# Kernel tuning notes

Measured on AMD Instinct MI355X. Metric: run time of the kernel, lower is better.

## Reference

```python
import jax, jax.numpy as jnp
import numpy as np

B, C, H, W = 4, 256, 48, 48
KD, NH, AR = 32, 8, 4
D = AR * KD            # 128, value dim per head
NHKD = NH * KD         # 256
DH = NH * D            # 1024
EPS = 1e-5


def _bn(y, g, b):
    # BN with fresh running stats (mean=0, var=1): y*g/sqrt(1+eps)+b, over channel dim
    s = g / jnp.sqrt(jnp.float32(1.0) + EPS)
    return y * s[None, :, None] + b[None, :, None]


def setup_inputs() -> dict:
    key = jax.random.key(0)
    ks = jax.random.split(key, 13)
    w = lambda k, sh: jax.random.normal(k, sh, jnp.float32) * 0.05
    g = lambda k, sh: 1.0 + jax.random.normal(k, sh, jnp.float32) * 0.05
    return {
        "x": jax.random.normal(ks[0], (B, C, H, W), jnp.float32),
        "wq": w(ks[1], (NHKD, C)), "gq": g(ks[2], (NHKD,)), "bq": w(ks[3], (NHKD,)),
        "wk": w(ks[4], (NHKD, C)), "gk": g(ks[5], (NHKD,)), "bk": w(ks[6], (NHKD,)),
        "wv": w(ks[7], (DH, C)),   "gv": g(ks[8], (DH,)),   "bv": w(ks[9], (DH,)),
        "wp": w(ks[10], (C, DH)),  "gp": g(ks[11], (C,)),   "bp": w(ks[12], (C,)),
    }


def reference(x, wq, gq, bq, wk, gk, bk, wv, gv, bv, wp, gp, bp):
    b, c, h, w = x.shape
    n = h * w
    xf = x.reshape(b, c, n)                                   # [B,C,N]
    # 1x1 conv == channel matmul, then BN
    q = _bn(jnp.einsum('oc,bcn->bon', wq, xf), gq, bq).reshape(b, NH, KD, n)
    k = _bn(jnp.einsum('oc,bcn->bon', wk, xf), gk, bk).reshape(b, NH, KD, n)
    v = _bn(jnp.einsum('oc,bcn->bon', wv, xf), gv, bv).reshape(b, NH, D, n)
    # NOTE: original forward does NOT apply self.scale
    attn = jax.nn.softmax(jnp.einsum('bhkn,bhkm->bhnm', q, k), axis=-1)  # [B,H,N,N]
    xx = jnp.einsum('bhnm,bhdm->bhdn', attn, v).reshape(b, DH, n)        # [B,DH,N]
    out = _bn(jnp.einsum('oc,bcn->bon', wp, jax.nn.relu(xx)), gp, bp)
    return out.reshape(b, c, h, w)
```

## Files before the change

### kernel.cpp

```cpp
#include <hip/hip_runtime.h>

#define BB 4
#define C 256
#define HW 2304
#define NH 8
#define KD 32
#define D 128
#define DH 1024
#define MQ 256

typedef unsigned short bf16u;
typedef __attribute__((ext_vector_type(8))) short short8;
typedef __attribute__((ext_vector_type(4))) short bfx4;
typedef __attribute__((ext_vector_type(4))) float f32x4;
typedef __attribute__((ext_vector_type(4))) unsigned ux4;
typedef __attribute__((ext_vector_type(2))) unsigned ux2;

union U8 { ux4 u; short8 s; };

__device__ __forceinline__ bf16u f2b(float f) {
    unsigned u = __float_as_uint(f);
    return (bf16u)((u + 0x7fffu + ((u >> 16) & 1u)) >> 16);
}
__device__ __forceinline__ unsigned pkb(float a, float b) {
    return __builtin_amdgcn_perm(__float_as_uint(b) + 0x8000u,
                                 __float_as_uint(a) + 0x8000u, 0x07060302u);
}

__device__ __forceinline__ void glds16(const bf16u* g, bf16u* l) {
    __builtin_amdgcn_global_load_lds(
        (const __attribute__((address_space(1))) unsigned int*)g,
        (__attribute__((address_space(3))) unsigned int*)l,
        16, 0, 0);
}

#define MFMA32 __builtin_amdgcn_mfma_f32_16x16x32_bf16

__global__ __launch_bounds__(256) void prepx(
    const float* __restrict__ wq, const float* __restrict__ wk, const float* __restrict__ wv,
    const float* __restrict__ gq, const float* __restrict__ bq,
    const float* __restrict__ gk, const float* __restrict__ bk,
    const float* __restrict__ gv, const float* __restrict__ bv,
    const float* __restrict__ x,
    bf16u* __restrict__ WcT, float* __restrict__ biasc, bf16u* __restrict__ xT)
{
    __shared__ float tile[64][68];
    const float rs = rsqrtf(1.0f + 1e-5f);
    const float L2E = 1.4426950408889634f;
    const int t = threadIdx.x, blk = blockIdx.x;
    if (blk < 192) {
        const int idx = (blk*256 + t) * 8;
        const int row = idx >> 8;
        const int k   = idx & 255;
        const float* src; float sc;
        if (row < 256)      { src = wq + idx;            sc = gq[row]*rs*L2E; }
        else if (row < 512) { src = wk + (idx - 65536);  sc = gk[row-256]*rs; }
        else                { src = wv + (idx - 131072); sc = gv[row-512]*rs; }
        float4 a = *(const float4*)(src);
        float4 c = *(const float4*)(src + 4);
        ux4 v;
        v.x = pkb(a.x*sc, a.y*sc); v.y = pkb(a.z*sc, a.w*sc);
        v.z = pkb(c.x*sc, c.y*sc); v.w = pkb(c.z*sc, c.w*sc);
        const size_t dst = (size_t)((row>>7)*8 + (k>>5))*4096
                         + (size_t)((row&127)*4 + ((k&31)>>3))*8;
        *(ux4*)(WcT + dst) = v;
    } else if (blk == 192) {
        #pragma unroll
        for (int kk = 0; kk < 6; ++kk) {
            const int r = kk*256 + t;
            float v;
            if (r < 256)      v = bq[r] * L2E;
            else if (r < 512) v = bk[r - 256];
            else              v = bv[r - 512];
            biasc[r] = v;
        }
    } else {
        const int idx = blk - 193;
        const int c0 = (idx & 3) * 64, n0 = ((idx >> 2) % 36) * 64, b = idx / 144;
        const float* xb = x + (size_t)b * C * HW;
        #pragma unroll
        for (int rr = 0; rr < 4; ++rr) {
            const int cl = rr*16 + (t >> 4);
            float4 v = *(const float4*)(xb + (size_t)(c0 + cl) * HW + n0 + (t & 15)*4);
            tile[cl][(t&15)*4+0] = v.x; tile[cl][(t&15)*4+1] = v.y;
            tile[cl][(t&15)*4+2] = v.z; tile[cl][(t&15)*4+3] = v.w;
        }
        __syncthreads();
        const int nl = t >> 2, ch = t & 3;
        short8 v0, v1;
        #pragma unroll
        for (int kk = 0; kk < 8; ++kk) v0[kk] = (short)f2b(tile[ch*16+kk][nl]);
        #pragma unroll
        for (int kk = 0; kk < 8; ++kk) v1[kk] = (short)f2b(tile[ch*16+8+kk][nl]);
        bf16u* dst = xT + ((size_t)b*HW + n0 + nl) * C + c0 + ch*16;
        *(short8*)(dst)     = v0;
        *(short8*)(dst + 8) = v1;
    }
}

__global__ __launch_bounds__(256, 3) void qkv_gemm(
    const bf16u* __restrict__ WcT, const float* __restrict__ biasc,
    const bf16u* __restrict__ xT,
    bf16u* __restrict__ qT, bf16u* __restrict__ kT, bf16u* __restrict__ vO)
{
    const int mt = blockIdx.x, ntb = blockIdx.y, b = blockIdx.z;
    const int r0 = mt * 128, c0 = ntb * 128;
    const int t = threadIdx.x, w = t >> 6, l = t & 63;
    const int l15 = l & 15, q = l >> 4;
    const int wr = w >> 1, wc = w & 1;

    __shared__ bf16u smem[24576];

    const bf16u* xb = xT + (size_t)b * HW * C;

    const int sA0 = w*128 + l, sA1 = w*128 + 64 + l;
    const bf16u* gA0 = WcT + (size_t)mt*32768 + (size_t)sA0*8;
    const bf16u* gA1 = WcT + (size_t)mt*32768 + (size_t)sA1*8;
    const bf16u* gB0 = xb + (size_t)(c0 + (sA0>>2)) * C + (sA0&3)*8;
    const bf16u* gB1 = xb + (size_t)(c0 + (sA1>>2)) * C + (sA1&3)*8;

    f32x4 acc[4][4];
    #pragma unroll
    for (int i = 0; i < 4; ++i)
        #pragma unroll
        for (int j = 0; j < 4; ++j) { acc[i][j][0]=0.f; acc[i][j][1]=0.f; acc[i][j][2]=0.f; acc[i][j][3]=0.f; }

    auto stage = [&](int it2, int bb) {
        bf16u* As = smem + bb*4096;
        bf16u* Bs = smem + 12288 + bb*4096;
        glds16(gA0 + it2*4096, As + sA0*8);
        glds16(gA1 + it2*4096, As + sA1*8);
        glds16(gB0 + it2*32,   Bs + sA0*8);
        glds16(gB1 + it2*32,   Bs + sA1*8);
    };

    const bool isV = (r0 >= 512);
    stage(0, 0); stage(1, 1);
    for (int it = 0; it < 8; ++it) {
        __syncthreads();
        if (it + 2 < 8) stage(it + 2, (it + 2) % 3);
        const bf16u* A = smem + (it % 3) * 4096;
        const bf16u* B = smem + 12288 + (it % 3) * 4096;
        short8 af[4], bf[4];
        #pragma unroll
        for (int i = 0; i < 4; ++i) af[i] = *(const short8*)(A + (wr*64 + i*16 + l15)*32 + q*8);
        #pragma unroll
        for (int j = 0; j < 4; ++j) bf[j] = *(const short8*)(B + (wc*64 + j*16 + l15)*32 + q*8);
        if (!isV) {
            #pragma unroll
            for (int i = 0; i < 4; ++i)
                #pragma unroll
                for (int j = 0; j < 4; ++j)
                    acc[i][j] = MFMA32(af[i], bf[j], acc[i][j], 0, 0, 0);
        } else {
            #pragma unroll
            for (int i = 0; i < 4; ++i)
                #pragma unroll
                for (int j = 0; j < 4; ++j)
                    acc[i][j] = MFMA32(bf[j], af[i], acc[i][j], 0, 0, 0);
        }
    }

    __syncthreads();
    bf16u* Od = smem + w * 4608;

    if (!isV) {
        float bC[4][4];
        #pragma unroll
        for (int i = 0; i < 4; ++i)
            #pragma unroll
            for (int r = 0; r < 4; ++r)
                bC[i][r] = biasc[r0 + wr*64 + i*16 + q*4 + r];
        #pragma unroll
        for (int i = 0; i < 4; ++i)
            #pragma unroll
            for (int j = 0; j < 4; ++j) {
                float y0 = acc[i][j][0] + bC[i][0];
                float y1 = acc[i][j][1] + bC[i][1];
                float y2 = acc[i][j][2] + bC[i][2];
                float y3 = acc[i][j][3] + bC[i][3];
                ux2 pk; pk.x = pkb(y0, y1); pk.y = pkb(y2, y3);
                *(ux2*)(Od + (j*16 + l15)*72 + i*16 + q*4) = pk;
            }
        bf16u* dst = (r0 < 256) ? qT : kT;
        #pragma unroll
        for (int hh = 0; hh < 2; ++hh) {
            const int h = ((r0 & 255) + wr*64 + hh*32) >> 5;
            bf16u* dh_ = dst + (size_t)(b*NH + h) * HW * KD;
            #pragma unroll
            for (int rg = 0; rg < 4; ++rg) {
                const int row = rg*16 + (l >> 2);
                const int n = c0 + wc*64 + row;
                short8 v = *(const short8*)(Od + row*72 + hh*32 + (l & 3)*8);
                *(short8*)(dh_ + (size_t)n * KD + (l & 3)*8) = v;
            }
        }
    } else {
        float bC[4];
        #pragma unroll
        for (int i = 0; i < 4; ++i)
            bC[i] = biasc[r0 + wr*64 + i*16 + l15];
        #pragma unroll
        for (int i = 0; i < 4; ++i)
            #pragma unroll
            for (int j = 0; j < 4; ++j) {
                float y0 = acc[i][j][0] + bC[i];
                float y1 = acc[i][j][1] + bC[i];
                float y2 = acc[i][j][2] + bC[i];
                float y3 = acc[i][j][3] + bC[i];
                ux2 pk; pk.x = pkb(y0, y1); pk.y = pkb(y2, y3);
                const int p = (j >> 1)*32 + q*8 + (j & 1)*4;
                *(ux2*)(Od + (i*16 + l15)*72 + p) = pk;
            }
        bf16u* dst = vO + (size_t)b * DH * HW;
        #pragma unroll
        for (int it2 = 0; it2 < 8; ++it2) {
            const int row = it2*8 + (l >> 3);
            const int d = (r0 - 512) + wr*64 + row;
            short8 v = *(const short8*)(Od + row*72 + (l & 7)*8);
            *(short8*)(dst + (size_t)d * HW + c0 + wc*64 + (l & 7)*8) = v;
        }
    }
}

__global__ __launch_bounds__(256, 3) void attn_mfma(
    const bf16u* __restrict__ qT, const bf16u* __restrict__ kT,
    const bf16u* __restrict__ vg, bf16u* __restrict__ xg)
{
    const int nt = blockIdx.x, h = blockIdx.y, b = blockIdx.z;
    const int n0 = nt * 128;
    const int t = threadIdx.x;
    const int w = t >> 6, l = t & 63, l15 = l & 15, q = l >> 4;

    const bf16u* qTh = qT + (size_t)(b*NH + h) * HW * KD;
    const bf16u* kTh = kT + (size_t)(b*NH + h) * HW * KD;
    const bf16u* vh  = vg + ((size_t)b*DH + (size_t)h*D) * HW;

    __shared__ bf16u smem[17408];

    short8 qf0 = *(const short8*)(qTh + (size_t)(n0 + w*32 +      l15) * KD + q*8);
    short8 qf1 = *(const short8*)(qTh + (size_t)(n0 + w*32 + 16 + l15) * KD + q*8);

    const short8 ones = { (short)0x3F80, (short)0x3F80, (short)0x3F80, (short)0x3F80,
                          (short)0x3F80, (short)0x3F80, (short)0x3F80, (short)0x3F80 };

    f32x4 o[2][8];
    #pragma unroll
    for (int a = 0; a < 2; ++a)
        #pragma unroll
        for (int d = 0; d < 8; ++d) { o[a][d][0]=0.f; o[a][d][1]=0.f; o[a][d][2]=0.f; o[a][d][3]=0.f; }
    f32x4 os0 = {0.f,0.f,0.f,0.f}, os1 = {0.f,0.f,0.f,0.f};
    const f32x4 zero = {0.f, 0.f, 0.f, 0.f};

    auto stageV = [&](int m0, int bb) {
        bf16u* Vs = smem + bb*8192;
        #pragma unroll
        for (int j = 0; j < 4; ++j) {
            const int s = (w*4 + j)*64 + l;
            const int d = s >> 3, c = s & 7, cg = c ^ (d & 7);
            glds16(vh + (size_t)d*HW + m0 + cg*8, Vs + (w*4 + j)*512);
        }
    };

    short8 kfc[4], kfn[4];
    #pragma unroll
    for (int kt = 0; kt < 4; ++kt)
        kfc[kt] = *(const short8*)(kTh + (size_t)(kt*16 + l15) * KD + q*8);
    stageV(0, 0);

    for (int mt = 0; mt < 36; ++mt) {
        __syncthreads();
        if (mt < 35) {
            stageV((mt+1)*64, (mt+1)&1);
            #pragma unroll
            for (int kt = 0; kt < 4; ++kt)
                kfn[kt] = *(const short8*)(kTh + (size_t)((mt+1)*64 + kt*16 + l15) * KD + q*8);
        }
        const bf16u* Vs = smem + (mt&1)*8192;

        f32x4 st0[4], st1[4];
        #pragma unroll
        for (int kt = 0; kt < 4; ++kt) {
            st0[kt] = MFMA32(kfc[kt], qf0, zero, 0, 0, 0);
            st1[kt] = MFMA32(kfc[kt], qf1, zero, 0, 0, 0);
        }

        unsigned dA0[4], dB0[4], dA1[4], dB1[4];
        #pragma unroll
        for (int kt = 0; kt < 4; ++kt) {
            float p0 = __builtin_amdgcn_exp2f(st0[kt][0]);
            float p1 = __builtin_amdgcn_exp2f(st0[kt][1]);
            float p2 = __builtin_amdgcn_exp2f(st0[kt][2]);
            float p3 = __builtin_amdgcn_exp2f(st0[kt][3]);
            dA0[kt] = pkb(p0, p1); dB0[kt] = pkb(p2, p3);
            float r0_ = __builtin_amdgcn_exp2f(st1[kt][0]);
            float r1_ = __builtin_amdgcn_exp2f(st1[kt][1]);
            float r2_ = __builtin_amdgcn_exp2f(st1[kt][2]);
            float r3_ = __builtin_amdgcn_exp2f(st1[kt][3]);
            dA1[kt] = pkb(r0_, r1_); dB1[kt] = pkb(r2_, r3_);
        }

        #pragma unroll
        for (int kh = 0; kh < 2; ++kh) {
            U8 u0, u1;
            u0.u[0] = dA0[kh*2];   u0.u[1] = dB0[kh*2];
            u0.u[2] = dA0[kh*2+1]; u0.u[3] = dB0[kh*2+1];
            u1.u[0] = dA1[kh*2];   u1.u[1] = dB1[kh*2];
            u1.u[2] = dA1[kh*2+1]; u1.u[3] = dB1[kh*2+1];
            #pragma unroll
            for (int dt = 0; dt < 8; ++dt) {
                const int d = dt*16 + l15;
                short8 vf = *(const short8*)(Vs + d*64 + (((kh*4 + q) ^ (d & 7)) * 8));
                o[0][dt] = MFMA32(u0.s, vf, o[0][dt], 0, 0, 0);
                o[1][dt] = MFMA32(u1.s, vf, o[1][dt], 0, 0, 0);
            }
            os0 = MFMA32(u0.s, ones, os0, 0, 0, 0);
            os1 = MFMA32(u1.s, ones, os1, 0, 0, 0);
        }

        if (mt < 35) {
            #pragma unroll
            for (int kt = 0; kt < 4; ++kt) kfc[kt] = kfn[kt];
        }
    }

    float inv0[4], inv1[4];
    #pragma unroll
    for (int r = 0; r < 4; ++r) {
        inv0[r] = 1.0f / os0[r];
        inv1[r] = 1.0f / os1[r];
    }
    __syncthreads();
    bf16u* Od = smem + w * 4352;
    #pragma unroll
    for (int dt = 0; dt < 8; ++dt)
        #pragma unroll
        for (int r = 0; r < 4; ++r) {
            float v0 = fmaxf(o[0][dt][r] * inv0[r], 0.f);
            float v1 = fmaxf(o[1][dt][r] * inv1[r], 0.f);
            Od[(     q*4 + r)*136 + dt*16 + l15] = f2b(v0);
            Od[(16 + q*4 + r)*136 + dt*16 + l15] = f2b(v1);
        }
    bf16u* xb = xg + ((size_t)b*HW + n0 + w*32) * DH + h*D;
    #pragma unroll
    for (int g = 0; g < 4; ++g) {
        const int row = g*8 + (l >> 3);
        #pragma unroll
        for (int hf = 0; hf < 2; ++hf) {
            const int ch = hf*8 + (l & 7);
            *(short8*)(xb + (size_t)row*DH + ch*8) =
                *(const short8*)(Od + row*136 + ch*8);
        }
    }
}

__global__ __launch_bounds__(256) void prep2(
    const float* __restrict__ wp, const float* __restrict__ gp,
    bf16u* __restrict__ WpT)
{
    const float rs = rsqrtf(1.0f + 1e-5f);
    const int item = blockIdx.x*256 + threadIdx.x;
    const int row = item >> 7;
    const int k   = (item & 127) * 8;
    const float sc = gp[row] * rs;
    const float* src = wp + (size_t)row*DH + k;
    float4 a = *(const float4*)(src);
    float4 c = *(const float4*)(src + 4);
    ux4 v;
    v.x = pkb(a.x*sc, a.y*sc); v.y = pkb(a.z*sc, a.w*sc);
    v.z = pkb(c.x*sc, c.y*sc); v.w = pkb(c.z*sc, c.w*sc);
    const size_t dst = (size_t)((row>>6)*16 + (k>>6))*4096
                     + (size_t)((row&63)*8 + ((k&63)>>3))*8;
    *(ux4*)(WpT + dst) = v;
}

__global__ __launch_bounds__(256, 3) void out_gemm(
    const bf16u* __restrict__ WpT, const float* __restrict__ bp,
    const bf16u* __restrict__ xx, float* __restrict__ out)
{
    const int mt = blockIdx.x, ntb = blockIdx.y, b = blockIdx.z;
    const int r0 = mt * 64, c0 = ntb * 64;
    const int t = threadIdx.x, w = t >> 6, l = t & 63;
    const int l15 = l & 15, q = l >> 4;
    const int wr = w >> 1, wc = w & 1;

    __shared__ bf16u smem[24576];

    const bf16u* xb = xx + (size_t)b * HW * DH;

    const int sA0 = t, sA1 = 256 + t;
    const bf16u* gA0 = WpT + (size_t)mt*65536 + (size_t)sA0*8;
    const bf16u* gA1 = WpT + (size_t)mt*65536 + (size_t)sA1*8;
    const int sB0 = w*128 + l, sB1 = w*128 + 64 + l;
    const bf16u* gB0 = xb + (size_t)(c0 + (sB0>>3)) * DH + (sB0&7)*8;
    const bf16u* gB1 = xb + (size_t)(c0 + (sB1>>3)) * DH + (sB1&7)*8;

    f32x4 acc[2][2];
    #pragma unroll
    for (int i = 0; i < 2; ++i)
        #pragma unroll
        for (int j = 0; j < 2; ++j) { acc[i][j][0]=0.f; acc[i][j][1]=0.f; acc[i][j][2]=0.f; acc[i][j][3]=0.f; }

    auto stage = [&](int it2, int bb) {
        bf16u* As = smem + bb*4096;
        bf16u* Bs = smem + 12288 + bb*4096;
        glds16(gA0 + it2*4096, As + sA0*8);
        glds16(gA1 + it2*4096, As + sA1*8);
        glds16(gB0 + it2*64,   Bs + sB0*8);
        glds16(gB1 + it2*64,   Bs + sB1*8);
    };

    stage(0, 0); stage(1, 1);
    for (int it = 0; it < 16; ++it) {
        __syncthreads();
        if (it + 2 < 16) stage(it + 2, (it + 2) % 3);
        const bf16u* A = smem + (it % 3) * 4096;
        const bf16u* B = smem + 12288 + (it % 3) * 4096;
        #pragma unroll
        for (int kk = 0; kk < 2; ++kk) {
            short8 af[2], bf[2];
            #pragma unroll
            for (int i = 0; i < 2; ++i) af[i] = *(const short8*)(A + (wr*32 + i*16 + l15)*64 + kk*32 + q*8);
            #pragma unroll
            for (int j = 0; j < 2; ++j) bf[j] = *(const short8*)(B + (wc*32 + j*16 + l15)*64 + kk*32 + q*8);
            #pragma unroll
            for (int i = 0; i < 2; ++i)
                #pragma unroll
                for (int j = 0; j < 2; ++j)
                    acc[i][j] = MFMA32(af[i], bf[j], acc[i][j], 0, 0, 0);
        }
    }

    #pragma unroll
    for (int i = 0; i < 2; ++i)
        #pragma unroll
        for (int r = 0; r < 4; ++r) {
            const int oc = r0 + wr*32 + i*16 + q*4 + r;
            const float bi = bp[oc];
            #pragma unroll
            for (int j = 0; j < 2; ++j) {
                const int n = c0 + wc*32 + j*16 + l15;
                out[((size_t)b*C + oc)*HW + n] = acc[i][j][r] + bi;
            }
        }
}

extern "C" void kernel_launch(void* const* d_in, const int* in_sizes, int n_in,
                              void* d_out, int out_size, void* d_ws, size_t ws_size,
                              hipStream_t stream) {
    const float* x  = (const float*)d_in[0];
    const float* wq = (const float*)d_in[1];
    const float* gq = (const float*)d_in[2];
    const float* bq = (const float*)d_in[3];
    const float* wk = (const float*)d_in[4];
    const float* gk = (const float*)d_in[5];
    const float* bk = (const float*)d_in[6];
    const float* wv = (const float*)d_in[7];
    const float* gv = (const float*)d_in[8];
    const float* bv = (const float*)d_in[9];
    const float* wp = (const float*)d_in[10];
    const float* gp = (const float*)d_in[11];
    const float* bp = (const float*)d_in[12];
    float* out = (float*)d_out;

    bf16u* qw = (bf16u*)d_ws;
    bf16u* kw = qw + (size_t)BB * MQ * HW;
    bf16u* vw = kw + (size_t)BB * MQ * HW;
    bf16u* xw = vw + (size_t)BB * DH * HW;
    bf16u* xTb = xw;
    bf16u* WcT = xw + (size_t)BB * MQ * HW;
    float* biasc = (float*)(WcT + 393216);
    bf16u* WpT = qw;

    hipLaunchKernelGGL(prepx, dim3(769), dim3(256), 0, stream,
                       wq, wk, wv, gq, bq, gk, bk, gv, bv, x, WcT, biasc, xTb);
    hipLaunchKernelGGL(qkv_gemm, dim3(12, 18, BB), dim3(256), 0, stream,
                       WcT, biasc, xTb, qw, kw, vw);
    hipLaunchKernelGGL(attn_mfma, dim3(18, NH, BB), dim3(256), 0, stream,
                       qw, kw, vw, xw);
    hipLaunchKernelGGL(prep2, dim3(128), dim3(256), 0, stream, wp, gp, WpT);
    hipLaunchKernelGGL(out_gemm, dim3(4, 36, BB), dim3(256), 0, stream,
                       WpT, bp, xw, out);
}
```

Measured before the change: 194.4 us.

## Retile attention to 2 waves with 48 query rows each, load Wp fragments directly

The attention kernel moves from 4 waves with 32 query rows each to 2 waves with 48 rows each. This gives a 96-query tile, 768 blocks and 128 threads per block, so each V tile loaded into LDS feeds more MFMAs per wave. The K fragment double buffer is replaced by loading the next K right after the exp stage. Separately, prep2 writes Wp in an MFMA-fragment-ready layout so out_gemm reads A fragments straight from global memory instead of staging them in LDS. The trade-offs are higher register pressure in attention and uncached global reads for A in the output GEMM.

```diff
diff --git a/kernel.cpp b/kernel.cpp
--- a/kernel.cpp
+++ b/kernel.cpp
@@ -11,7 +11,6 @@
 
 typedef unsigned short bf16u;
 typedef __attribute__((ext_vector_type(8))) short short8;
-typedef __attribute__((ext_vector_type(4))) short bfx4;
 typedef __attribute__((ext_vector_type(4))) float f32x4;
 typedef __attribute__((ext_vector_type(4))) unsigned ux4;
 typedef __attribute__((ext_vector_type(2))) unsigned ux2;
@@ -223,12 +222,12 @@
     }
 }
 
-__global__ __launch_bounds__(256, 3) void attn_mfma(
+__global__ __launch_bounds__(128, 2) void attn_mfma(
     const bf16u* __restrict__ qT, const bf16u* __restrict__ kT,
     const bf16u* __restrict__ vg, bf16u* __restrict__ xg)
 {
     const int nt = blockIdx.x, h = blockIdx.y, b = blockIdx.z;
-    const int n0 = nt * 128;
+    const int n0 = nt * 96;
     const int t = threadIdx.x;
     const int w = t >> 6, l = t & 63, l15 = l & 15, q = l >> 4;
 
@@ -236,33 +235,37 @@
     const bf16u* kTh = kT + (size_t)(b*NH + h) * HW * KD;
     const bf16u* vh  = vg + ((size_t)b*DH + (size_t)h*D) * HW;
 
-    __shared__ bf16u smem[17408];
-
-    short8 qf0 = *(const short8*)(qTh + (size_t)(n0 + w*32 +      l15) * KD + q*8);
-    short8 qf1 = *(const short8*)(qTh + (size_t)(n0 + w*32 + 16 + l15) * KD + q*8);
+    __shared__ bf16u smem[16384];
+
+    short8 qf[3];
+    #pragma unroll
+    for (int g = 0; g < 3; ++g)
+        qf[g] = *(const short8*)(qTh + (size_t)(n0 + w*48 + g*16 + l15) * KD + q*8);
 
     const short8 ones = { (short)0x3F80, (short)0x3F80, (short)0x3F80, (short)0x3F80,
                           (short)0x3F80, (short)0x3F80, (short)0x3F80, (short)0x3F80 };
 
-    f32x4 o[2][8];
-    #pragma unroll
-    for (int a = 0; a < 2; ++a)
-        #pragma unroll
-        for (int d = 0; d < 8; ++d) { o[a][d][0]=0.f; o[a][d][1]=0.f; o[a][d][2]=0.f; o[a][d][3]=0.f; }
-    f32x4 os0 = {0.f,0.f,0.f,0.f}, os1 = {0.f,0.f,0.f,0.f};
+    f32x4 o[3][8];
+    #pragma unroll
+    for (int g = 0; g < 3; ++g)
+        #pragma unroll
+        for (int d = 0; d < 8; ++d) { o[g][d][0]=0.f; o[g][d][1]=0.f; o[g][d][2]=0.f; o[g][d][3]=0.f; }
+    f32x4 os[3];
+    #pragma unroll
+    for (int g = 0; g < 3; ++g) { os[g][0]=0.f; os[g][1]=0.f; os[g][2]=0.f; os[g][3]=0.f; }
     const f32x4 zero = {0.f, 0.f, 0.f, 0.f};
 
     auto stageV = [&](int m0, int bb) {
         bf16u* Vs = smem + bb*8192;
         #pragma unroll
-        for (int j = 0; j < 4; ++j) {
-            const int s = (w*4 + j)*64 + l;
+        for (int j = 0; j < 8; ++j) {
+            const int s = (w*8 + j)*64 + l;
             const int d = s >> 3, c = s & 7, cg = c ^ (d & 7);
-            glds16(vh + (size_t)d*HW + m0 + cg*8, Vs + (w*4 + j)*512);
+            glds16(vh + (size_t)d*HW + m0 + cg*8, Vs + (w*8 + j)*512);
         }
     };
 
-    short8 kfc[4], kfn[4];
+    short8 kfc[4];
     #pragma unroll
     for (int kt = 0; kt < 4; ++kt)
         kfc[kt] = *(const short8*)(kTh + (size_t)(kt*16 + l15) * KD + q*8);
@@ -270,81 +273,75 @@
 
     for (int mt = 0; mt < 36; ++mt) {
         __syncthreads();
+        if (mt < 35) stageV((mt+1)*64, (mt+1)&1);
+        const bf16u* Vs = smem + (mt&1)*8192;
+
+        unsigned dA[3][4], dB[3][4];
+        #pragma unroll
+        for (int g = 0; g < 3; ++g) {
+            f32x4 st[4];
+            #pragma unroll
+            for (int kt = 0; kt < 4; ++kt)
+                st[kt] = MFMA32(kfc[kt], qf[g], zero, 0, 0, 0);
+            #pragma unroll
+            for (int kt = 0; kt < 4; ++kt) {
+                float p0 = __builtin_amdgcn_exp2f(st[kt][0]);
+                float p1 = __builtin_amdgcn_exp2f(st[kt][1]);
+                float p2 = __builtin_amdgcn_exp2f(st[kt][2]);
+                float p3 = __builtin_amdgcn_exp2f(st[kt][3]);
+                dA[g][kt] = pkb(p0, p1); dB[g][kt] = pkb(p2, p3);
+            }
+        }
+
         if (mt < 35) {
-            stageV((mt+1)*64, (mt+1)&1);
             #pragma unroll
             for (int kt = 0; kt < 4; ++kt)
-                kfn[kt] = *(const short8*)(kTh + (size_t)((mt+1)*64 + kt*16 + l15) * KD + q*8);
-        }
-        const bf16u* Vs = smem + (mt&1)*8192;
-
-        f32x4 st0[4], st1[4];
-        #pragma unroll
-        for (int kt = 0; kt < 4; ++kt) {
-            st0[kt] = MFMA32(kfc[kt], qf0, zero, 0, 0, 0);
-            st1[kt] = MFMA32(kfc[kt], qf1, zero, 0, 0, 0);
-        }
-
-        unsigned dA0[4], dB0[4], dA1[4], dB1[4];
-        #pragma unroll
-        for (int kt = 0; kt < 4; ++kt) {
-            float p0 = __builtin_amdgcn_exp2f(st0[kt][0]);
-            float p1 = __builtin_amdgcn_exp2f(st0[kt][1]);
-            float p2 = __builtin_amdgcn_exp2f(st0[kt][2]);
-            float p3 = __builtin_amdgcn_exp2f(st0[kt][3]);
-            dA0[kt] = pkb(p0, p1); dB0[kt] = pkb(p2, p3);
-            float r0_ = __builtin_amdgcn_exp2f(st1[kt][0]);
-            float r1_ = __builtin_amdgcn_exp2f(st1[kt][1]);
-            float r2_ = __builtin_amdgcn_exp2f(st1[kt][2]);
-            float r3_ = __builtin_amdgcn_exp2f(st1[kt][3]);
-            dA1[kt] = pkb(r0_, r1_); dB1[kt] = pkb(r2_, r3_);
+                kfc[kt] = *(const short8*)(kTh + (size_t)((mt+1)*64 + kt*16 + l15) * KD + q*8);
         }
 
         #pragma unroll
         for (int kh = 0; kh < 2; ++kh) {
-            U8 u0, u1;
-            u0.u[0] = dA0[kh*2];   u0.u[1] = dB0[kh*2];
-            u0.u[2] = dA0[kh*2+1]; u0.u[3] = dB0[kh*2+1];
-            u1.u[0] = dA1[kh*2];   u1.u[1] = dB1[kh*2];
-            u1.u[2] = dA1[kh*2+1]; u1.u[3] = dB1[kh*2+1];
+            U8 u[3];
+            #pragma unroll
+            for (int g = 0; g < 3; ++g) {
+                u[g].u[0] = dA[g][kh*2];   u[g].u[1] = dB[g][kh*2];
+                u[g].u[2] = dA[g][kh*2+1]; u[g].u[3] = dB[g][kh*2+1];
+            }
             #pragma unroll
             for (int dt = 0; dt < 8; ++dt) {
                 const int d = dt*16 + l15;
                 short8 vf = *(const short8*)(Vs + d*64 + (((kh*4 + q) ^ (d & 7)) * 8));
-                o[0][dt] = MFMA32(u0.s, vf, o[0][dt], 0, 0, 0);
-                o[1][dt] = MFMA32(u1.s, vf, o[1][dt], 0, 0, 0);
-            }
-            os0 = MFMA32(u0.s, ones, os0, 0, 0, 0);
-            os1 = MFMA32(u1.s, ones, os1, 0, 0, 0);
-        }
-
-        if (mt < 35) {
-            #pragma unroll
-            for (int kt = 0; kt < 4; ++kt) kfc[kt] = kfn[kt];
-        }
-    }
-
-    float inv0[4], inv1[4];
-    #pragma unroll
-    for (int r = 0; r < 4; ++r) {
-        inv0[r] = 1.0f / os0[r];
-        inv1[r] = 1.0f / os1[r];
-    }
+                #pragma unroll
+                for (int g = 0; g < 3; ++g)
+                    o[g][dt] = MFMA32(u[g].s, vf, o[g][dt], 0, 0, 0);
+            }
+            #pragma unroll
+            for (int g = 0; g < 3; ++g)
+                os[g] = MFMA32(u[g].s, ones, os[g], 0, 0, 0);
+        }
+    }
+
+    float inv[3][4];
+    #pragma unroll
+    for (int g = 0; g < 3; ++g)
+        #pragma unroll
+        for (int r = 0; r < 4; ++r)
+            inv[g][r] = 1.0f / os[g][r];
     __syncthreads();
-    bf16u* Od = smem + w * 4352;
-    #pragma unroll
-    for (int dt = 0; dt < 8; ++dt)
-        #pragma unroll
-        for (int r = 0; r < 4; ++r) {
-            float v0 = fmaxf(o[0][dt][r] * inv0[r], 0.f);
-            float v1 = fmaxf(o[1][dt][r] * inv1[r], 0.f);
-            Od[(     q*4 + r)*136 + dt*16 + l15] = f2b(v0);
-            Od[(16 + q*4 + r)*136 + dt*16 + l15] = f2b(v1);
-        }
-    bf16u* xb = xg + ((size_t)b*HW + n0 + w*32) * DH + h*D;
-    #pragma unroll
-    for (int g = 0; g < 4; ++g) {
-        const int row = g*8 + (l >> 3);
+    bf16u* Od = smem + w * 6528;
+    #pragma unroll
+    for (int g = 0; g < 3; ++g)
+        #pragma unroll
+        for (int dt = 0; dt < 8; ++dt)
+            #pragma unroll
+            for (int r = 0; r < 4; ++r) {
+                float v = fmaxf(o[g][dt][r] * inv[g][r], 0.f);
+                Od[(g*16 + q*4 + r)*136 + dt*16 + l15] = f2b(v);
+            }
+    bf16u* xb = xg + ((size_t)b*HW + n0 + w*48) * DH + h*D;
+    #pragma unroll
+    for (int it = 0; it < 6; ++it) {
+        const int row = it*8 + (l >> 3);
         #pragma unroll
         for (int hf = 0; hf < 2; ++hf) {
             const int ch = hf*8 + (l & 7);
@@ -369,8 +366,8 @@
     ux4 v;
     v.x = pkb(a.x*sc, a.y*sc); v.y = pkb(a.z*sc, a.w*sc);
     v.z = pkb(c.x*sc, c.y*sc); v.w = pkb(c.z*sc, c.w*sc);
-    const size_t dst = (size_t)((row>>6)*16 + (k>>6))*4096
-                     + (size_t)((row&63)*8 + ((k&63)>>3))*8;
+    const size_t dst = (size_t)((row>>4)*32 + (k>>5))*512
+                     + (size_t)(((k>>3)&3)*16 + (row&15))*8;
     *(ux4*)(WpT + dst) = v;
 }
 
@@ -384,16 +381,14 @@
     const int l15 = l & 15, q = l >> 4;
     const int wr = w >> 1, wc = w & 1;
 
-    __shared__ bf16u smem[24576];
+    __shared__ bf16u smem[12288];
 
     const bf16u* xb = xx + (size_t)b * HW * DH;
 
-    const int sA0 = t, sA1 = 256 + t;
-    const bf16u* gA0 = WpT + (size_t)mt*65536 + (size_t)sA0*8;
-    const bf16u* gA1 = WpT + (size_t)mt*65536 + (size_t)sA1*8;
     const int sB0 = w*128 + l, sB1 = w*128 + 64 + l;
     const bf16u* gB0 = xb + (size_t)(c0 + (sB0>>3)) * DH + (sB0&7)*8;
     const bf16u* gB1 = xb + (size_t)(c0 + (sB1>>3)) * DH + (sB1&7)*8;
+    const bf16u* gA  = WpT + (size_t)(mt*4 + wr*2)*32*512 + (size_t)l*8;
 
     f32x4 acc[2][2];
     #pragma unroll
@@ -402,27 +397,25 @@
         for (int j = 0; j < 2; ++j) { acc[i][j][0]=0.f; acc[i][j][1]=0.f; acc[i][j][2]=0.f; acc[i][j][3]=0.f; }
 
     auto stage = [&](int it2, int bb) {
-        bf16u* As = smem + bb*4096;
-        bf16u* Bs = smem + 12288 + bb*4096;
-        glds16(gA0 + it2*4096, As + sA0*8);
-        glds16(gA1 + it2*4096, As + sA1*8);
-        glds16(gB0 + it2*64,   Bs + sB0*8);
-        glds16(gB1 + it2*64,   Bs + sB1*8);
+        bf16u* Bs = smem + bb*4096;
+        glds16(gB0 + it2*64, Bs + sB0*8);
+        glds16(gB1 + it2*64, Bs + sB1*8);
     };
 
     stage(0, 0); stage(1, 1);
     for (int it = 0; it < 16; ++it) {
         __syncthreads();
         if (it + 2 < 16) stage(it + 2, (it + 2) % 3);
-        const bf16u* A = smem + (it % 3) * 4096;
-        const bf16u* B = smem + 12288 + (it % 3) * 4096;
+        const bf16u* B = smem + (it % 3) * 4096;
         #pragma unroll
         for (int kk = 0; kk < 2; ++kk) {
             short8 af[2], bf[2];
             #pragma unroll
-            for (int i = 0; i < 2; ++i) af[i] = *(const short8*)(A + (wr*32 + i*16 + l15)*64 + kk*32 + q*8);
-            #pragma unroll
-            for (int j = 0; j < 2; ++j) bf[j] = *(const short8*)(B + (wc*32 + j*16 + l15)*64 + kk*32 + q*8);
+            for (int i = 0; i < 2; ++i)
+                af[i] = *(const short8*)(gA + (size_t)(i*32 + it*2 + kk)*512);
+            #pragma unroll
+            for (int j = 0; j < 2; ++j)
+                bf[j] = *(const short8*)(B + (wc*32 + j*16 + l15)*64 + kk*32 + q*8);
             #pragma unroll
             for (int i = 0; i < 2; ++i)
                 #pragma unroll
@@ -476,7 +469,7 @@
                        wq, wk, wv, gq, bq, gk, bk, gv, bv, x, WcT, biasc, xTb);
     hipLaunchKernelGGL(qkv_gemm, dim3(12, 18, BB), dim3(256), 0, stream,
                        WcT, biasc, xTb, qw, kw, vw);
-    hipLaunchKernelGGL(attn_mfma, dim3(18, NH, BB), dim3(256), 0, stream,
+    hipLaunchKernelGGL(attn_mfma, dim3(24, NH, BB), dim3(128), 0, stream,
                        qw, kw, vw, xw);
     hipLaunchKernelGGL(prep2, dim3(128), dim3(256), 0, stream, wp, gp, WpT);
     hipLaunchKernelGGL(out_gemm, dim3(4, 36, BB), dim3(256), 0, stream,
```

After: 192.4 us, median of 2. Within noise of the previous version (-1.0%).
